# Performance work log

Hardware: AMD Instinct MI355X
Metric: run time of the kernel (lower is better)

The kernel has to match this reference:

```python
import jax, jax.numpy as jnp
import numpy as np

CHUNK = 64  # chunk size for chunkwise delta-rule


def l2norm(x, eps=1e-6):
    return x * jax.lax.rsqrt(jnp.sum(x * x, axis=-1, keepdims=True) + eps)


def delta_rule_chunked(q, k, v, beta):
    """Chunkwise-parallel DeltaNet delta rule.

    Recurrence (per head): S_t = S_{t-1} + k_t u_t^T with
      u_t = beta_t * (v_t - S_{t-1}^T k_t),   o_t = S_t^T q_t.
    q,k,v: [B,H,L,D]; beta: [B,H,L]. Returns o: [B,H,L,D].
    """
    B, H, L, D = q.shape
    n = L // CHUNK
    def to_chunks(t):
        return jnp.moveaxis(t.reshape(B, H, n, CHUNK, *t.shape[4:] if t.ndim > 4 else ()) if False else t.reshape(B, H, n, CHUNK, -1) if t.ndim == 4 else t.reshape(B, H, n, CHUNK), 2, 0)
    qc = jnp.moveaxis(q.reshape(B, H, n, CHUNK, D), 2, 0)  # [n,B,H,C,D]
    kc = jnp.moveaxis(k.reshape(B, H, n, CHUNK, D), 2, 0)
    vc = jnp.moveaxis(v.reshape(B, H, n, CHUNK, D), 2, 0)
    bc = jnp.moveaxis(beta.reshape(B, H, n, CHUNK), 2, 0)   # [n,B,H,C]
    strict = jnp.tril(jnp.ones((CHUNK, CHUNK), bool), -1)
    incl = jnp.tril(jnp.ones((CHUNK, CHUNK), bool))
    eye = jnp.eye(CHUNK, dtype=q.dtype)

    def step(S, inp):
        qi, ki, vi, bi = inp  # [B,H,C,D], [B,H,C]
        kk = jnp.einsum('bhid,bhjd->bhij', ki, ki)            # [B,H,C,C]
        # Unit lower-triangular system (I + B*strict_tril(K K^T)) U = B*(V - K S)
        T = eye + jnp.where(strict, bi[..., :, None] * kk, 0.0)
        rhs = bi[..., None] * (vi - jnp.einsum('bhcd,bhde->bhce', ki, S))
        U = jax.scipy.linalg.solve_triangular(T, rhs, lower=True)
        qk = jnp.einsum('bhid,bhjd->bhij', qi, ki)
        O = jnp.einsum('bhcd,bhde->bhce', qi, S) \
            + jnp.einsum('bhij,bhje->bhie', jnp.where(incl, qk, 0.0), U)
        S_new = S + jnp.einsum('bhcd,bhce->bhde', ki, U)      # [B,H,D,D]
        return S_new, O

    S0 = jnp.zeros((B, H, D, D), q.dtype)
    _, O = jax.lax.scan(step, S0, (qc, kc, vc, bc))
    return jnp.moveaxis(O, 0, 2).reshape(B, H, L, D)


def setup_inputs() -> dict:
    key = jax.random.key(0)
    ks = jax.random.split(key, 7)
    B, C, Hh, Ww = 8, 768, 64, 64
    n_heads = 12
    s = 1.0 / np.sqrt(C)
    x = jax.random.normal(ks[0], (B, C, Hh, Ww), jnp.float32)
    Wq = jax.random.normal(ks[1], (C, C), jnp.float32) * s
    Wk = jax.random.normal(ks[2], (C, C), jnp.float32) * s
    Wv = jax.random.normal(ks[3], (C, C), jnp.float32) * s
    Wb = jax.random.normal(ks[4], (C, n_heads), jnp.float32) * s
    Wo = jax.random.normal(ks[5], (C, C), jnp.float32) * s
    return {"x": x, "Wq": Wq, "Wk": Wk, "Wv": Wv, "Wb": Wb, "Wo": Wo}


def reference(x, Wq, Wk, Wv, Wb, Wo):
    B, C, Hh, Ww = x.shape
    L = Hh * Ww
    n_heads = Wb.shape[1]
    D = C // n_heads
    t = x.reshape(B, C, L).transpose(0, 2, 1)                 # [B,L,C] tokens
    def heads(z):
        return z.reshape(B, L, n_heads, D).transpose(0, 2, 1, 3)  # [B,H,L,D]
    q = l2norm(heads(jax.nn.silu(t @ Wq)))
    k = l2norm(heads(jax.nn.silu(t @ Wk)))
    v = heads(jax.nn.silu(t @ Wv))
    beta = jax.nn.sigmoid(t @ Wb).transpose(0, 2, 1)          # [B,H,L]
    o = delta_rule_chunked(q, k, v, beta)                     # [B,H,L,D]
    o = o.transpose(0, 2, 1, 3).reshape(B, L, C)
    y = o @ Wo
    out = t + y                                               # residual
    return out.transpose(0, 2, 1).reshape(B, C, Hh, Ww)
```

## Files before the change

### kernel.cpp

```cpp
#include <hip/hip_runtime.h>


#define B_  8
#define C_  768
#define L_  4096
#define NH_ 12
#define D_  64
#define NC_ 64
#define BH_ 96

typedef unsigned short ushort_t;
typedef float f32x4 __attribute__((ext_vector_type(4)));
typedef unsigned short u16x4 __attribute__((ext_vector_type(4)));
typedef unsigned short u16x8 __attribute__((ext_vector_type(8)));
using short8 = __attribute__((ext_vector_type(8))) short;

__device__ __forceinline__ float b2f(ushort_t u) {
  union { unsigned u; float f; } x; x.u = ((unsigned)u) << 16; return x.f;
}
__device__ __forceinline__ ushort_t f2b(float f) {
  union { float f; unsigned u; } x; x.f = f;
  unsigned r = (x.u + 0x7FFFu + ((x.u >> 16) & 1u)) >> 16;
  return (ushort_t)r;
}
__device__ __forceinline__ f32x4 mfma16(short8 a, short8 b, f32x4 c) {
  return __builtin_amdgcn_mfma_f32_16x16x32_bf16(a, b, c, 0, 0, 0);
}
__device__ __forceinline__ void gload16(const ushort_t* g, ushort_t* l) {
  __builtin_amdgcn_global_load_lds(
      (const __attribute__((address_space(1))) void*)(g),
      (__attribute__((address_space(3))) void*)(l), 16, 0, 0);
}

#define SWZ(e, i) (((e) * 64) + ((i) ^ (((e) & 7) << 3)))

__global__ __launch_bounds__(256) void k_wprep(
    const float* __restrict__ W, ushort_t* __restrict__ hi,
    ushort_t* __restrict__ lo) {
  __shared__ float ts[64 * 65];
  int tid = threadIdx.x;
  int c0 = blockIdx.x * 64;
  int n0 = blockIdx.y * 64;
  #pragma unroll
  for (int it = 0; it < 4; ++it) {
    int e = tid + it * 256;
    int r = e >> 4, c4 = (e & 15) * 4;
    *(f32x4*)&ts[r * 65 + c4] =
        *(const f32x4*)(W + (size_t)(c0 + r) * C_ + n0 + c4);
  }
  __syncthreads();
  #pragma unroll
  for (int it = 0; it < 4; ++it) {
    int e = tid + it * 256;
    int n = e >> 4, r4 = (e & 15) * 4;
    u16x4 hv, lv;
    #pragma unroll
    for (int q = 0; q < 4; ++q) {
      float w = ts[(r4 + q) * 65 + n];
      ushort_t h = f2b(w);
      hv[q] = h;
      lv[q] = f2b(w - b2f(h));
    }
    *(u16x4*)(hi + (size_t)(n0 + n) * C_ + c0 + r4) = hv;
    *(u16x4*)(lo + (size_t)(n0 + n) * C_ + c0 + r4) = lv;
  }
}

__global__ __launch_bounds__(256) void k_xtr(
    const float* __restrict__ x, ushort_t* __restrict__ hi,
    ushort_t* __restrict__ lo) {
  __shared__ float ts[64 * 65];
  int tid = threadIdx.x;
  int l0 = blockIdx.x * 64;
  int c0 = blockIdx.y * 64;
  int b = blockIdx.z;
  const float* xb = x + (size_t)b * C_ * L_;
  #pragma unroll
  for (int it = 0; it < 4; ++it) {
    int e = tid + it * 256;
    int ci = e >> 4, l4 = (e & 15) * 4;
    *(f32x4*)&ts[ci * 65 + l4] =
        *(const f32x4*)(xb + (size_t)(c0 + ci) * L_ + l0 + l4);
  }
  __syncthreads();
  #pragma unroll
  for (int it = 0; it < 4; ++it) {
    int e = tid + it * 256;
    int li = e >> 4, c4 = (e & 15) * 4;
    u16x4 hv, lv;
    #pragma unroll
    for (int q = 0; q < 4; ++q) {
      float w = ts[(c4 + q) * 65 + li];
      ushort_t h = f2b(w);
      hv[q] = h;
      lv[q] = f2b(w - b2f(h));
    }
    size_t base = ((size_t)b * L_ + l0 + li) * C_ + c0 + c4;
    *(u16x4*)(hi + base) = hv;
    *(u16x4*)(lo + base) = lv;
  }
}

__global__ __launch_bounds__(256) void k_beta(
    const float* __restrict__ x, const float* __restrict__ Wb,
    float* __restrict__ beta) {
  __shared__ float wb[C_ * NH_];
  int tid = threadIdx.x;
  for (int i = tid; i < C_ * NH_; i += 256) wb[i] = Wb[i];
  __syncthreads();
  int b = blockIdx.y;
  int l = blockIdx.x * 256 + tid;
  f32x4 a0 = {0.f, 0.f, 0.f, 0.f}, a1 = a0, a2 = a0;
  const float* xb = x + (size_t)b * C_ * L_ + l;
  for (int c = 0; c < C_; ++c) {
    float xv = xb[(size_t)c * L_];
    const f32x4* wr = (const f32x4*)&wb[c * NH_];
    a0 += xv * wr[0]; a1 += xv * wr[1]; a2 += xv * wr[2];
  }
  float* bp = beta + (size_t)b * NH_ * L_ + l;
  #pragma unroll
  for (int h = 0; h < 4; ++h) {
    bp[(size_t)h * L_]       = 1.f / (1.f + expf(-a0[h]));
    bp[(size_t)(h + 4) * L_] = 1.f / (1.f + expf(-a1[h]));
    bp[(size_t)(h + 8) * L_] = 1.f / (1.f + expf(-a2[h]));
  }
}

__global__ __launch_bounds__(512, 2) void k_qkv8(
    const ushort_t* __restrict__ xhi, const ushort_t* __restrict__ xlo,
    const ushort_t* __restrict__ whi, const ushort_t* __restrict__ wlo,
    ushort_t* __restrict__ qout, ushort_t* __restrict__ kout,
    ushort_t* __restrict__ vout) {
  __shared__ __align__(16) ushort_t LA[2][256 * 64];
  __shared__ __align__(16) ushort_t LB[2][256 * 64];
  int tid = threadIdx.x;
  int bid = blockIdx.x;
  int swz = (bid & 7) * 144 + (bid >> 3);
  int bx = swz & 127, by = swz >> 7;
  int row0 = bx * 256, n0 = by * 256;
  int wid = tid >> 6, lane = tid & 63;
  int wm = wid >> 2, wn = wid & 3;
  int lr = lane & 15, lk = lane >> 4;
  int m7 = lr & 7;
  int aofs[4], bofs[4];
  #pragma unroll
  for (int j = 0; j < 4; ++j) {
    int u = tid + j * 512;
    int r = u >> 3, s = (u & 7) ^ (r & 7);
    aofs[j] = (row0 + r) * C_ + s * 8;
    bofs[j] = (n0 + r) * C_ + s * 8;
  }
  f32x4 acc[8][4];
  #pragma unroll
  for (int mf = 0; mf < 8; ++mf)
    #pragma unroll
    for (int nf = 0; nf < 4; ++nf) acc[mf][nf] = (f32x4){0.f, 0.f, 0.f, 0.f};
  #pragma unroll
  for (int j = 0; j < 4; ++j) {
    gload16(xhi + aofs[j], &LA[0][(tid + j * 512) * 8]);
    gload16(whi + bofs[j], &LB[0][(tid + j * 512) * 8]);
  }
  __syncthreads();
  #pragma unroll 1
  for (int t = 0; t < 36; ++t) {
    int bb = t & 1, nb = bb ^ 1;
    int tt = t + 1;
    bool st = (tt < 36);
    int seg = tt / 12;
    int kseg = (tt - seg * 12) * 64;
    const ushort_t* Asrc = (seg == 1) ? xlo : xhi;
    const ushort_t* Bsrc = (seg == 2) ? wlo : whi;
    short8 bF[4][2];
    #pragma unroll
    for (int q = 0; q < 4; ++q) {
      short8 aF[2][2];
      int ra0 = wm * 128 + q * 32 + lr;
      int ra1 = ra0 + 16;
      #pragma unroll
      for (int ks = 0; ks < 2; ++ks) {
        int g = ks * 4 + lk;
        aF[0][ks] = *(const short8*)&LA[bb][(ra0 * 8 + (g ^ m7)) * 8];
        aF[1][ks] = *(const short8*)&LA[bb][(ra1 * 8 + (g ^ m7)) * 8];
      }
      if (q == 0) {
        #pragma unroll
        for (int nf = 0; nf < 4; ++nf) {
          int rb = wn * 64 + nf * 16 + lr;
          #pragma unroll
          for (int ks = 0; ks < 2; ++ks) {
            int g = ks * 4 + lk;
            bF[nf][ks] = *(const short8*)&LB[bb][(rb * 8 + (g ^ m7)) * 8];
          }
        }
      }
      if (st) {
        if (q == 0) {
          gload16(Asrc + kseg + aofs[0], &LA[nb][(tid) * 8]);
          gload16(Asrc + kseg + aofs[1], &LA[nb][(tid + 512) * 8]);
          gload16(Asrc + kseg + aofs[2], &LA[nb][(tid + 1024) * 8]);
          gload16(Asrc + kseg + aofs[3], &LA[nb][(tid + 1536) * 8]);
        }
        if (q == 1) {
          gload16(Bsrc + kseg + bofs[0], &LB[nb][(tid) * 8]);
          gload16(Bsrc + kseg + bofs[1], &LB[nb][(tid + 512) * 8]);
        }
        if (q == 2) {
          gload16(Bsrc + kseg + bofs[2], &LB[nb][(tid + 1024) * 8]);
          gload16(Bsrc + kseg + bofs[3], &LB[nb][(tid + 1536) * 8]);
        }
      }
      __builtin_amdgcn_s_barrier();
      asm volatile("s_waitcnt lgkmcnt(0)" ::: "memory");
      __builtin_amdgcn_sched_barrier(0);
      __builtin_amdgcn_s_setprio(1);
      #pragma unroll
      for (int nf = 0; nf < 4; ++nf) {
        acc[2 * q][nf]     = mfma16(aF[0][0], bF[nf][0], acc[2 * q][nf]);
        acc[2 * q][nf]     = mfma16(aF[0][1], bF[nf][1], acc[2 * q][nf]);
        acc[2 * q + 1][nf] = mfma16(aF[1][0], bF[nf][0], acc[2 * q + 1][nf]);
        acc[2 * q + 1][nf] = mfma16(aF[1][1], bF[nf][1], acc[2 * q + 1][nf]);
      }
      __builtin_amdgcn_s_setprio(0);
      if (q == 3) asm volatile("s_waitcnt vmcnt(0)" ::: "memory");
      __builtin_amdgcn_s_barrier();
    }
  }
  #pragma unroll
  for (int mf = 0; mf < 8; ++mf)
    #pragma unroll
    for (int nf = 0; nf < 4; ++nf)
      #pragma unroll
      for (int rr = 0; rr < 4; ++rr) {
        float xv = acc[mf][nf][rr];
        acc[mf][nf][rr] = xv / (1.f + expf(-xv));
      }
  int colbase = n0 + wn * 64;
  int proj = colbase / 768;
  if (proj < 2) {
    #pragma unroll
    for (int mf = 0; mf < 8; ++mf)
      #pragma unroll
      for (int rr = 0; rr < 4; ++rr) {
        float ss = 0.f;
        #pragma unroll
        for (int nf = 0; nf < 4; ++nf) ss += acc[mf][nf][rr] * acc[mf][nf][rr];
        ss += __shfl_xor(ss, 1); ss += __shfl_xor(ss, 2);
        ss += __shfl_xor(ss, 4); ss += __shfl_xor(ss, 8);
        float rs = rsqrtf(ss + 1e-6f);
        #pragma unroll
        for (int nf = 0; nf < 4; ++nf) acc[mf][nf][rr] *= rs;
      }
  }
  ushort_t* outsel = (proj == 0) ? qout : ((proj == 1) ? kout : vout);
  int h = (colbase - proj * 768) >> 6;
  #pragma unroll
  for (int mf = 0; mf < 8; ++mf) {
    int row = row0 + wm * 128 + mf * 16 + lk * 4;
    int b = row >> 12, l = row & 4095;
    ushort_t* op0 = outsel + (((size_t)b * NH_ + h) * L_ + l) * 64;
    #pragma unroll
    for (int nf = 0; nf < 4; ++nf) {
      int d = nf * 16 + lr;
      #pragma unroll
      for (int rr = 0; rr < 4; ++rr)
        op0[(size_t)rr * 64 + d] = f2b(acc[mf][nf][rr]);
    }
  }
}

__global__ __launch_bounds__(256) void k_pre2(
    const ushort_t* __restrict__ qg, ushort_t* kg, ushort_t* vg,
    const float* __restrict__ betag, ushort_t* __restrict__ kwg,
    ushort_t* __restrict__ aqg) {
  __shared__ float As[64 * 68];
  __shared__ float XK[64 * 68];
  __shared__ float XV[64 * 68];
  int tid = threadIdx.x;
  int nc = blockIdx.x, bh = blockIdx.y;
  const size_t cb = ((size_t)bh * 64 + nc) * 4096;
  const float* bb = betag + (size_t)bh * L_ + nc * 64;
  int wid = tid >> 6, lane = tid & 63;
  int lr = lane & 15, lk = lane >> 4;
  short8 kbf[4][2], ka[2], qa[2];
  #pragma unroll
  for (int nf = 0; nf < 4; ++nf)
    #pragma unroll
    for (int ks = 0; ks < 2; ++ks)
      kbf[nf][ks] = *(const short8*)(kg + cb +
          (size_t)(nf * 16 + lr) * 64 + ks * 32 + lk * 8);
  #pragma unroll
  for (int ks = 0; ks < 2; ++ks) {
    ka[ks] = *(const short8*)(kg + cb + (size_t)(wid * 16 + lr) * 64 + ks * 32 + lk * 8);
    qa[ks] = *(const short8*)(qg + cb + (size_t)(wid * 16 + lr) * 64 + ks * 32 + lk * 8);
  }
  f32x4 kk[4], qk[4];
  #pragma unroll
  for (int nf = 0; nf < 4; ++nf) {
    kk[nf] = (f32x4){0.f, 0.f, 0.f, 0.f};
    qk[nf] = (f32x4){0.f, 0.f, 0.f, 0.f};
    kk[nf] = mfma16(ka[0], kbf[nf][0], kk[nf]);
    kk[nf] = mfma16(ka[1], kbf[nf][1], kk[nf]);
    qk[nf] = mfma16(qa[0], kbf[nf][0], qk[nf]);
    qk[nf] = mfma16(qa[1], kbf[nf][1], qk[nf]);
  }
  float bi[4];
  #pragma unroll
  for (int r = 0; r < 4; ++r) bi[r] = bb[wid * 16 + lk * 4 + r];
  #pragma unroll
  for (int r = 0; r < 4; ++r) {
    int i = wid * 16 + lk * 4 + r;
    #pragma unroll
    for (int nf = 0; nf < 4; ++nf) {
      int j = nf * 16 + lr;
      As[i * 68 + j] = (j < i) ? bi[r] * kk[nf][r] : 0.f;
      aqg[cb + (size_t)i * 64 + j] = (j <= i) ? f2b(qk[nf][r]) : (ushort_t)0;
    }
  }
  #pragma unroll
  for (int it = 0; it < 2; ++it) {
    int e = tid + it * 256;
    int i = e >> 3, c0 = (e & 7) * 8;
    float bv = bb[i];
    u16x8 kv8 = *(const u16x8*)(kg + cb + (size_t)i * 64 + c0);
    u16x8 vv8 = *(const u16x8*)(vg + cb + (size_t)i * 64 + c0);
    f32x4 klo = {bv*b2f(kv8[0]), bv*b2f(kv8[1]), bv*b2f(kv8[2]), bv*b2f(kv8[3])};
    f32x4 khi = {bv*b2f(kv8[4]), bv*b2f(kv8[5]), bv*b2f(kv8[6]), bv*b2f(kv8[7])};
    f32x4 vlo = {bv*b2f(vv8[0]), bv*b2f(vv8[1]), bv*b2f(vv8[2]), bv*b2f(vv8[3])};
    f32x4 vhi = {bv*b2f(vv8[4]), bv*b2f(vv8[5]), bv*b2f(vv8[6]), bv*b2f(vv8[7])};
    *(f32x4*)&XK[i * 68 + c0]     = klo;
    *(f32x4*)&XK[i * 68 + c0 + 4] = khi;
    *(f32x4*)&XV[i * 68 + c0]     = vlo;
    *(f32x4*)&XV[i * 68 + c0 + 4] = vhi;
  }
  __syncthreads();
  if (tid < 128) {
    float* Xc = (tid < 64) ? (XK + tid) : (XV + (tid - 64));
    float xr[32];
    #pragma unroll
    for (int i = 0; i < 32; ++i) xr[i] = Xc[i * 68];
    #pragma unroll
    for (int i = 1; i < 32; ++i) {
      float xi = xr[i];
      #pragma unroll
      for (int jb = 0; jb <= (i >> 2); ++jb) {
        f32x4 a4 = *(const f32x4*)&As[i * 68 + jb * 4];
        xi -= a4[0]*xr[jb*4] + a4[1]*xr[jb*4+1] + a4[2]*xr[jb*4+2] + a4[3]*xr[jb*4+3];
      }
      xr[i] = xi;
    }
    #pragma unroll
    for (int i = 1; i < 32; ++i) Xc[i * 68] = xr[i];
  } else {
    int ks = wid - 2;
    #pragma unroll
    for (int nf = 0; nf < 4; ++nf)
      #pragma unroll
      for (int jj = 0; jj < 8; ++jj) {
        int d = ks * 32 + lk * 8 + jj;
        kg[cb + (size_t)d * 64 + nf * 16 + lr] = (ushort_t)kbf[nf][ks][jj];
      }
  }
  __syncthreads();
  if (tid >= 128) {
    int col = tid - 128;
    float* Xc = (col < 64) ? (XK + col) : (XV + (col - 64));
    float xr[32];
    #pragma unroll
    for (int i = 0; i < 32; ++i) xr[i] = Xc[(32 + i) * 68];
    #pragma unroll
    for (int jb = 0; jb < 8; ++jb) {
      float xt0 = Xc[(jb*4+0)*68], xt1 = Xc[(jb*4+1)*68];
      float xt2 = Xc[(jb*4+2)*68], xt3 = Xc[(jb*4+3)*68];
      #pragma unroll
      for (int i = 0; i < 32; ++i) {
        f32x4 a4 = *(const f32x4*)&As[(32 + i) * 68 + jb * 4];
        xr[i] -= a4[0]*xt0 + a4[1]*xt1 + a4[2]*xt2 + a4[3]*xt3;
      }
    }
    #pragma unroll
    for (int i = 1; i < 32; ++i) {
      float xi = xr[i];
      #pragma unroll
      for (int jb = 8; jb <= ((32 + i) >> 2); ++jb) {
        f32x4 a4 = *(const f32x4*)&As[(32 + i) * 68 + jb * 4];
        xi -= a4[0]*xr[jb*4-32] + a4[1]*xr[jb*4-31]
            + a4[2]*xr[jb*4-30] + a4[3]*xr[jb*4-29];
      }
      xr[i] = xi;
    }
    #pragma unroll
    for (int i = 0; i < 32; ++i) Xc[(32 + i) * 68] = xr[i];
  } else {
    #pragma unroll
    for (int it = 0; it < 4; ++it) {
      int u = tid + it * 128;
      int i = u >> 4, d0 = (u & 15) * 4;
      f32x4 v4 = *(const f32x4*)&XK[i * 68 + d0];
      u16x4 pk = {f2b(v4[0]), f2b(v4[1]), f2b(v4[2]), f2b(v4[3])};
      *(u16x4*)(kwg + cb + (size_t)i * 64 + d0) = pk;
      f32x4 w4 = *(const f32x4*)&XV[i * 68 + d0];
      u16x4 pv = {f2b(w4[0]), f2b(w4[1]), f2b(w4[2]), f2b(w4[3])};
      *(u16x4*)(vg + cb + (size_t)i * 64 + d0) = pv;
    }
  }
  __syncthreads();
  #pragma unroll
  for (int it = 0; it < 2; ++it) {
    int u = tid + it * 256;
    int i = 32 + (u >> 4), d0 = (u & 15) * 4;
    f32x4 v4 = *(const f32x4*)&XK[i * 68 + d0];
    u16x4 pk = {f2b(v4[0]), f2b(v4[1]), f2b(v4[2]), f2b(v4[3])};
    *(u16x4*)(kwg + cb + (size_t)i * 64 + d0) = pk;
    f32x4 w4 = *(const f32x4*)&XV[i * 68 + d0];
    u16x4 pv = {f2b(w4[0]), f2b(w4[1]), f2b(w4[2]), f2b(w4[3])};
    *(u16x4*)(vg + cb + (size_t)i * 64 + d0) = pv;
  }
}

__global__ __launch_bounds__(256) void k_seq(
    const ushort_t* __restrict__ qg,  const ushort_t* __restrict__ ktg,
    const ushort_t* __restrict__ kwg, const ushort_t* __restrict__ vwg,
    const ushort_t* __restrict__ aqg, ushort_t* __restrict__ og) {
  __shared__ float    STs[64 * 64];
  __shared__ ushort_t SbT[64 * 64];
  __shared__ ushort_t UT [64 * 64];
  int tid = threadIdx.x, bh = blockIdx.x;
  int w  = tid >> 6, l = tid & 63;
  int lr = l & 15, lk = l >> 4;
  int mrow = w * 16 + lr;
  int r0   = w * 16 + lk * 4;
  for (int i = tid; i < 4096; i += 256) { STs[i] = 0.f; SbT[i] = 0; }
  int b = bh / NH_, h = bh % NH_;
  ushort_t* ob = og + (size_t)b * L_ * C_ + h * 64;
  __syncthreads();
  for (int nc = 0; nc < NC_; ++nc) {
    const size_t cb = ((size_t)bh * 64 + nc) * 4096;
    const ushort_t* Kw = kwg + cb;
    const ushort_t* Qc = qg  + cb;
    const ushort_t* Aq = aqg + cb;
    const ushort_t* KT = ktg + cb;
    const ushort_t* Vw = vwg + cb;
    short8 a_kw0 = *(const short8*)(Kw + mrow * 64 + lk * 8);
    short8 a_kw1 = *(const short8*)(Kw + mrow * 64 + 32 + lk * 8);
    short8 a_q0  = *(const short8*)(Qc + mrow * 64 + lk * 8);
    short8 a_q1  = *(const short8*)(Qc + mrow * 64 + 32 + lk * 8);
    short8 a_aq0 = *(const short8*)(Aq + mrow * 64 + lk * 8);
    short8 a_aq1 = *(const short8*)(Aq + mrow * 64 + 32 + lk * 8);
    short8 a_kt0 = *(const short8*)(KT + mrow * 64 + lk * 8);
    short8 a_kt1 = *(const short8*)(KT + mrow * 64 + 32 + lk * 8);
    float vwv[4][4];
    #pragma unroll
    for (int t = 0; t < 4; ++t)
      #pragma unroll
      for (int r = 0; r < 4; ++r)
        vwv[t][r] = b2f(Vw[(size_t)(r0 + r) * 64 + t * 16 + lr]);
    #pragma unroll
    for (int t = 0; t < 4; ++t) {
      int e = t * 16 + lr;
      f32x4 acc = {0.f, 0.f, 0.f, 0.f};
      short8 b0 = *(const short8*)(SbT + SWZ(e, lk * 8));
      short8 b1 = *(const short8*)(SbT + SWZ(e, 32 + lk * 8));
      acc = mfma16(a_kw0, b0, acc);
      acc = mfma16(a_kw1, b1, acc);
      u16x4 uo;
      #pragma unroll
      for (int r = 0; r < 4; ++r) uo[r] = f2b(vwv[t][r] - acc[r]);
      *(u16x4*)(UT + SWZ(e, r0)) = uo;
    }
    __syncthreads();
    #pragma unroll
    for (int t = 0; t < 4; ++t) {
      int e = t * 16 + lr;
      f32x4 acc = {0.f, 0.f, 0.f, 0.f};
      short8 s0 = *(const short8*)(SbT + SWZ(e, lk * 8));
      short8 s1 = *(const short8*)(SbT + SWZ(e, 32 + lk * 8));
      short8 u0 = *(const short8*)(UT  + SWZ(e, lk * 8));
      short8 u1 = *(const short8*)(UT  + SWZ(e, 32 + lk * 8));
      acc = mfma16(a_q0,  s0, acc);
      acc = mfma16(a_q1,  s1, acc);
      acc = mfma16(a_aq0, u0, acc);
      acc = mfma16(a_aq1, u1, acc);
      #pragma unroll
      for (int r = 0; r < 4; ++r)
        ob[(size_t)(nc * 64 + r0 + r) * C_ + e] = f2b(acc[r]);
    }
    __syncthreads();
    #pragma unroll
    for (int t = 0; t < 4; ++t) {
      int e = t * 16 + lr;
      f32x4 acc = {0.f, 0.f, 0.f, 0.f};
      short8 u0 = *(const short8*)(UT + SWZ(e, lk * 8));
      short8 u1 = *(const short8*)(UT + SWZ(e, 32 + lk * 8));
      acc = mfma16(a_kt0, u0, acc);
      acc = mfma16(a_kt1, u1, acc);
      float* sp = &STs[SWZ(e, r0)];
      f32x4 sv = *(const f32x4*)sp;
      sv += acc;
      *(f32x4*)sp = sv;
      u16x4 sb = {f2b(sv[0]), f2b(sv[1]), f2b(sv[2]), f2b(sv[3])};
      *(u16x4*)(SbT + SWZ(e, r0)) = sb;
    }
    __syncthreads();
  }
}

__global__ __launch_bounds__(256) void k_final2(
    const ushort_t* __restrict__ o, const ushort_t* __restrict__ wot,
    const float* __restrict__ x, float* __restrict__ outp) {
  __shared__ __align__(16) ushort_t Ats[128 * 32];
  __shared__ __align__(16) ushort_t Bts[128 * 32];
  int tid = threadIdx.x;
  int b = blockIdx.z;
  int c0 = blockIdx.y * 128;
  int l0 = blockIdx.x * 128;
  int wid = tid >> 6, lane = tid & 63;
  int lr = lane & 15, lk = lane >> 4;
  f32x4 acc[2][8];
  #pragma unroll
  for (int mf = 0; mf < 2; ++mf)
    #pragma unroll
    for (int nf = 0; nf < 8; ++nf) acc[mf][nf] = (f32x4){0.f, 0.f, 0.f, 0.f};
  const ushort_t* ga = wot + (size_t)c0 * C_;
  const ushort_t* gb = o + ((size_t)b * L_ + l0) * C_;
  int ra0 = wid * 32 + lr, ra1 = wid * 32 + 16 + lr;
  int ua0 = ra0 * 4 + (lk ^ ((ra0 >> 1) & 3));
  int ua1 = ra1 * 4 + (lk ^ ((ra1 >> 1) & 3));
  for (int kb = 0; kb < C_; kb += 32) {
    if (kb) __syncthreads();
    #pragma unroll
    for (int c = 0; c < 2; ++c) {
      int u = tid + c * 256;
      int r = u >> 2, sp = u & 3;
      int s = sp ^ ((r >> 1) & 3);
      size_t goff = (size_t)r * C_ + kb + s * 8;
      gload16(ga + goff, &Ats[u * 8]);
      gload16(gb + goff, &Bts[u * 8]);
    }
    __syncthreads();
    short8 a0 = *(const short8*)&Ats[ua0 * 8];
    short8 a1 = *(const short8*)&Ats[ua1 * 8];
    #pragma unroll
    for (int nf = 0; nf < 8; ++nf) {
      int rb = nf * 16 + lr;
      int ub = rb * 4 + (lk ^ ((rb >> 1) & 3));
      short8 bv = *(const short8*)&Bts[ub * 8];
      acc[0][nf] = mfma16(a0, bv, acc[0][nf]);
      acc[1][nf] = mfma16(a1, bv, acc[1][nf]);
    }
  }
  #pragma unroll
  for (int mf = 0; mf < 2; ++mf) {
    int cc0 = c0 + wid * 32 + mf * 16 + lk * 4;
    #pragma unroll
    for (int nf = 0; nf < 8; ++nf) {
      int ll = l0 + nf * 16 + lr;
      #pragma unroll
      for (int rr = 0; rr < 4; ++rr) {
        size_t idx = ((size_t)b * C_ + cc0 + rr) * L_ + ll;
        outp[idx] = acc[mf][nf][rr] + x[idx];
      }
    }
  }
}

extern "C" void kernel_launch(void* const* d_in, const int* in_sizes, int n_in,
                              void* d_out, int out_size, void* d_ws, size_t ws_size,
                              hipStream_t stream) {
  (void)in_sizes; (void)n_in; (void)out_size; (void)ws_size;
  const float* x  = (const float*)d_in[0];
  const float* Wq = (const float*)d_in[1];
  const float* Wk = (const float*)d_in[2];
  const float* Wv = (const float*)d_in[3];
  const float* Wb = (const float*)d_in[4];
  const float* Wo = (const float*)d_in[5];
  float* outp = (float*)d_out;

  const size_t NE = (size_t)B_ * NH_ * L_ * D_;
  const size_t WE = (size_t)C_ * C_;
  ushort_t* q    = (ushort_t*)d_ws;
  ushort_t* kbuf = q + NE;
  ushort_t* v    = kbuf + NE;
  float*    beta = (float*)(v + NE);
  ushort_t* o    = (ushort_t*)(beta + (size_t)B_ * NH_ * L_);
  ushort_t* kw   = o + NE;
  ushort_t* aqk  = kw + NE;
  ushort_t* wt   = aqk + NE;
  ushort_t* xt_hi = aqk;
  ushort_t* xt_lo = kw;
  ushort_t* wt_q = wt, *wt_o = wt + 3 * WE;
  ushort_t* wl_q = o;

  k_wprep<<<dim3(12, 12), 256, 0, stream>>>(Wq, wt_q, wl_q);
  k_wprep<<<dim3(12, 12), 256, 0, stream>>>(Wk, wt + WE, o + WE);
  k_wprep<<<dim3(12, 12), 256, 0, stream>>>(Wv, wt + 2 * WE, o + 2 * WE);
  k_wprep<<<dim3(12, 12), 256, 0, stream>>>(Wo, wt_o, o + 3 * WE);
  k_xtr<<<dim3(L_ / 64, C_ / 64, B_), 256, 0, stream>>>(x, xt_hi, xt_lo);
  k_beta<<<dim3(L_ / 256, B_), 256, 0, stream>>>(x, Wb, beta);
  k_qkv8<<<dim3((B_ * L_ / 256) * (2304 / 256)), 512, 0, stream>>>(
      xt_hi, xt_lo, wt_q, wl_q, q, kbuf, v);
  k_pre2<<<dim3(NC_, BH_), 256, 0, stream>>>(q, kbuf, v, beta, kw, aqk);
  k_seq<<<dim3(BH_), 256, 0, stream>>>(q, kbuf, kw, v, aqk, o);
  k_final2<<<dim3(L_ / 128, C_ / 128, B_), 256, 0, stream>>>(o, wt_o, x, outp);
}
```

Measured before the change: 1.099 ms.

## Deepen QKV GEMM LDS pipeline to four stages with K=32 slices

The fused QKV projection GEMM now uses a 4-slot ring of half-size (K=32) LDS tiles, prefetching three stages ahead with counted vmcnt waits instead of double buffering K=64 tiles with a full vmcnt(0) drain each iteration. The swizzle is changed to match the 4-chunk row layout. The aim is to hide global-load latency better and avoid stalling on every tile. In exchange it runs twice as many loop iterations and barriers, and the hand-tuned vmcnt counts are fragile.

```diff
diff --git a/kernel.cpp b/kernel.cpp
--- a/kernel.cpp
+++ b/kernel.cpp
@@ -131,8 +131,8 @@
     const ushort_t* __restrict__ whi, const ushort_t* __restrict__ wlo,
     ushort_t* __restrict__ qout, ushort_t* __restrict__ kout,
     ushort_t* __restrict__ vout) {
-  __shared__ __align__(16) ushort_t LA[2][256 * 64];
-  __shared__ __align__(16) ushort_t LB[2][256 * 64];
+  __shared__ __align__(16) ushort_t LA[4][256 * 32];
+  __shared__ __align__(16) ushort_t LB[4][256 * 32];
   int tid = threadIdx.x;
   int bid = blockIdx.x;
   int swz = (bid & 7) * 144 + (bid >> 3);
@@ -141,14 +141,14 @@
   int wid = tid >> 6, lane = tid & 63;
   int wm = wid >> 2, wn = wid & 3;
   int lr = lane & 15, lk = lane >> 4;
-  int m7 = lr & 7;
-  int aofs[4], bofs[4];
-  #pragma unroll
-  for (int j = 0; j < 4; ++j) {
+  int aoff[2], boff[2];
+  #pragma unroll
+  for (int j = 0; j < 2; ++j) {
     int u = tid + j * 512;
-    int r = u >> 3, s = (u & 7) ^ (r & 7);
-    aofs[j] = (row0 + r) * C_ + s * 8;
-    bofs[j] = (n0 + r) * C_ + s * 8;
+    int r = u >> 2, sp = u & 3;
+    int s4 = sp ^ ((r >> 1) & 3);
+    aoff[j] = (row0 + r) * C_ + s4 * 8;
+    boff[j] = (n0 + r) * C_ + s4 * 8;
   }
   f32x4 acc[8][4];
   #pragma unroll
@@ -156,72 +156,68 @@
     #pragma unroll
     for (int nf = 0; nf < 4; ++nf) acc[mf][nf] = (f32x4){0.f, 0.f, 0.f, 0.f};
   #pragma unroll
-  for (int j = 0; j < 4; ++j) {
-    gload16(xhi + aofs[j], &LA[0][(tid + j * 512) * 8]);
-    gload16(whi + bofs[j], &LB[0][(tid + j * 512) * 8]);
-  }
-  __syncthreads();
+  for (int ss = 0; ss < 3; ++ss) {
+    gload16(xhi + aoff[0] + ss * 32, &LA[ss][tid * 8]);
+    gload16(xhi + aoff[1] + ss * 32, &LA[ss][(tid + 512) * 8]);
+    gload16(whi + boff[0] + ss * 32, &LB[ss][tid * 8]);
+    gload16(whi + boff[1] + ss * 32, &LB[ss][(tid + 512) * 8]);
+  }
+  asm volatile("s_waitcnt vmcnt(8)" ::: "memory");
+  __builtin_amdgcn_s_barrier();
   #pragma unroll 1
-  for (int t = 0; t < 36; ++t) {
-    int bb = t & 1, nb = bb ^ 1;
-    int tt = t + 1;
-    bool st = (tt < 36);
-    int seg = tt / 12;
-    int kseg = (tt - seg * 12) * 64;
-    const ushort_t* Asrc = (seg == 1) ? xlo : xhi;
-    const ushort_t* Bsrc = (seg == 2) ? wlo : whi;
-    short8 bF[4][2];
-    #pragma unroll
-    for (int q = 0; q < 4; ++q) {
-      short8 aF[2][2];
-      int ra0 = wm * 128 + q * 32 + lr;
-      int ra1 = ra0 + 16;
-      #pragma unroll
-      for (int ks = 0; ks < 2; ++ks) {
-        int g = ks * 4 + lk;
-        aF[0][ks] = *(const short8*)&LA[bb][(ra0 * 8 + (g ^ m7)) * 8];
-        aF[1][ks] = *(const short8*)&LA[bb][(ra1 * 8 + (g ^ m7)) * 8];
-      }
-      if (q == 0) {
+  for (int s = 0; s < 72; ++s) {
+    int slot = s & 3;
+    int t = s + 3;
+    bool st = (t < 72);
+    int tseg = t / 24;
+    int tk = (t - tseg * 24) * 32;
+    const ushort_t* Asrc = (tseg == 1) ? xlo : xhi;
+    const ushort_t* Bsrc = (tseg == 2) ? wlo : whi;
+    int nslot = t & 3;
+    short8 bF[4];
+    #pragma unroll
+    for (int ph = 0; ph < 2; ++ph) {
+      short8 aF[4];
+      #pragma unroll
+      for (int m = 0; m < 4; ++m) {
+        int ra = wm * 128 + (ph * 4 + m) * 16 + lr;
+        int ua = ra * 4 + (lk ^ ((ra >> 1) & 3));
+        aF[m] = *(const short8*)&LA[slot][ua * 8];
+      }
+      if (ph == 0) {
         #pragma unroll
         for (int nf = 0; nf < 4; ++nf) {
           int rb = wn * 64 + nf * 16 + lr;
-          #pragma unroll
-          for (int ks = 0; ks < 2; ++ks) {
-            int g = ks * 4 + lk;
-            bF[nf][ks] = *(const short8*)&LB[bb][(rb * 8 + (g ^ m7)) * 8];
-          }
+          int ub = rb * 4 + (lk ^ ((rb >> 1) & 3));
+          bF[nf] = *(const short8*)&LB[slot][ub * 8];
         }
-      }
-      if (st) {
-        if (q == 0) {
-          gload16(Asrc + kseg + aofs[0], &LA[nb][(tid) * 8]);
-          gload16(Asrc + kseg + aofs[1], &LA[nb][(tid + 512) * 8]);
-          gload16(Asrc + kseg + aofs[2], &LA[nb][(tid + 1024) * 8]);
-          gload16(Asrc + kseg + aofs[3], &LA[nb][(tid + 1536) * 8]);
+        if (st) {
+          gload16(Asrc + aoff[0] + tk, &LA[nslot][tid * 8]);
+          gload16(Asrc + aoff[1] + tk, &LA[nslot][(tid + 512) * 8]);
         }
-        if (q == 1) {
-          gload16(Bsrc + kseg + bofs[0], &LB[nb][(tid) * 8]);
-          gload16(Bsrc + kseg + bofs[1], &LB[nb][(tid + 512) * 8]);
-        }
-        if (q == 2) {
-          gload16(Bsrc + kseg + bofs[2], &LB[nb][(tid + 1024) * 8]);
-          gload16(Bsrc + kseg + bofs[3], &LB[nb][(tid + 1536) * 8]);
-        }
+      } else if (st) {
+        gload16(Bsrc + boff[0] + tk, &LB[nslot][tid * 8]);
+        gload16(Bsrc + boff[1] + tk, &LB[nslot][(tid + 512) * 8]);
       }
       __builtin_amdgcn_s_barrier();
       asm volatile("s_waitcnt lgkmcnt(0)" ::: "memory");
       __builtin_amdgcn_sched_barrier(0);
       __builtin_amdgcn_s_setprio(1);
       #pragma unroll
-      for (int nf = 0; nf < 4; ++nf) {
-        acc[2 * q][nf]     = mfma16(aF[0][0], bF[nf][0], acc[2 * q][nf]);
-        acc[2 * q][nf]     = mfma16(aF[0][1], bF[nf][1], acc[2 * q][nf]);
-        acc[2 * q + 1][nf] = mfma16(aF[1][0], bF[nf][0], acc[2 * q + 1][nf]);
-        acc[2 * q + 1][nf] = mfma16(aF[1][1], bF[nf][1], acc[2 * q + 1][nf]);
-      }
+      for (int nf = 0; nf < 4; ++nf)
+        #pragma unroll
+        for (int m = 0; m < 4; ++m)
+          acc[ph * 4 + m][nf] = mfma16(aF[m], bF[nf], acc[ph * 4 + m][nf]);
       __builtin_amdgcn_s_setprio(0);
-      if (q == 3) asm volatile("s_waitcnt vmcnt(0)" ::: "memory");
+      if (ph == 1) {
+        if (s < 69) {
+          asm volatile("s_waitcnt vmcnt(8)" ::: "memory");
+        } else if (s == 69) {
+          asm volatile("s_waitcnt vmcnt(4)" ::: "memory");
+        } else if (s == 70) {
+          asm volatile("s_waitcnt vmcnt(0)" ::: "memory");
+        }
+      }
       __builtin_amdgcn_s_barrier();
     }
   }
```

Result: slower. 1.162 ms (+5.8%).
